# Optimization experiments

Measured on AMD Instinct MI355X. Metric: run time of the kernel, lower is better.

Reference implementation:

```python
import jax, jax.numpy as jnp
import numpy as np

HIDDEN = 2048
N_HEADS = 16
N_KV_HEADS = 4
HEAD_DIM = HIDDEN // N_HEADS  # 128
WINDOW = 2048
ROPE_THETA = 10000.0


def setup_inputs() -> dict:
    key = jax.random.key(0)
    ks = jax.random.split(key, 5)
    B, S = 1, 4096
    scale = 0.02
    return {
        "hidden_states": jax.random.normal(ks[0], (B, S, HIDDEN), dtype=jnp.float32),
        # nn.Linear weights are [out_features, in_features]
        "q_w": jax.random.normal(ks[1], (N_HEADS * HEAD_DIM, HIDDEN), dtype=jnp.float32) * scale,
        "k_w": jax.random.normal(ks[2], (N_KV_HEADS * HEAD_DIM, HIDDEN), dtype=jnp.float32) * scale,
        "v_w": jax.random.normal(ks[3], (N_KV_HEADS * HEAD_DIM, HIDDEN), dtype=jnp.float32) * scale,
        "o_w": jax.random.normal(ks[4], (HIDDEN, N_HEADS * HEAD_DIM), dtype=jnp.float32) * scale,
    }


def _rope_cos_sin(seq_len, dtype):
    inv_freq = 1.0 / (ROPE_THETA ** (jnp.arange(0, HEAD_DIM, 2, dtype=jnp.float32) / HEAD_DIM))
    pos = jnp.arange(seq_len, dtype=jnp.float32)
    freqs = pos[:, None] * inv_freq[None, :]          # [S, D/2]
    emb = jnp.concatenate([freqs, freqs], axis=-1)    # [S, D]
    return jnp.cos(emb).astype(dtype), jnp.sin(emb).astype(dtype)


def _rotate_half(x):
    x1, x2 = jnp.split(x, 2, axis=-1)
    return jnp.concatenate([-x2, x1], axis=-1)


def reference(hidden_states, q_w, k_w, v_w, o_w):
    B, S, _ = hidden_states.shape
    dtype = hidden_states.dtype

    q = hidden_states @ q_w.T                         # [B,S,H*D]
    k = hidden_states @ k_w.T                         # [B,S,Hkv*D]
    v = hidden_states @ v_w.T

    q = q.reshape(B, S, N_HEADS, HEAD_DIM).transpose(0, 2, 1, 3)      # [B,H,S,D]
    k = k.reshape(B, S, N_KV_HEADS, HEAD_DIM).transpose(0, 2, 1, 3)   # [B,Hkv,S,D]
    v = v.reshape(B, S, N_KV_HEADS, HEAD_DIM).transpose(0, 2, 1, 3)

    cos, sin = _rope_cos_sin(S, dtype)                # [S,D]
    cos = cos[None, None]
    sin = sin[None, None]
    q = q * cos + _rotate_half(q) * sin
    k = k * cos + _rotate_half(k) * sin

    n_rep = N_HEADS // N_KV_HEADS
    k = jnp.repeat(k, n_rep, axis=1)                  # [B,H,S,D]
    v = jnp.repeat(v, n_rep, axis=1)

    scores = jnp.einsum("bhqd,bhkd->bhqk", q, k) / jnp.sqrt(jnp.array(HEAD_DIM, dtype))

    pos = jnp.arange(S)
    rel = pos[:, None] - pos[None, :]
    allowed = (rel >= 0) & (rel < WINDOW)             # causal sliding window
    mask = jnp.where(allowed, jnp.array(0.0, dtype), jnp.array(-jnp.inf, dtype))
    scores = scores + mask[None, None]

    attn = jax.nn.softmax(scores.astype(jnp.float32), axis=-1).astype(dtype)

    out = jnp.einsum("bhqk,bhkd->bhqd", attn, v)      # [B,H,S,D]
    out = out.transpose(0, 2, 1, 3).reshape(B, S, N_HEADS * HEAD_DIM)
    return out @ o_w.T
```

## Files before the change

### kernel.cpp

```cpp
#include <hip/hip_runtime.h>
#include <stdint.h>

typedef unsigned short u16;
typedef unsigned int u32;
typedef float f32x4 __attribute__((ext_vector_type(4)));
typedef float f32x8 __attribute__((ext_vector_type(8)));
typedef int   i32x4 __attribute__((ext_vector_type(4)));
typedef __bf16 bf16x8 __attribute__((ext_vector_type(8)));
typedef u16 u16x4 __attribute__((ext_vector_type(4)));

constexpr int S_LEN = 4096;
constexpr int HID   = 2048;
constexpr int WIN   = 2048;

__device__ __forceinline__ u32 f2bf_u(float f) {
  u32 u = __builtin_bit_cast(u32, f);
  return (u + 0x7fffu + ((u >> 16) & 1u)) >> 16;
}
__device__ __forceinline__ float bf2f(u16 u) {
  return __builtin_bit_cast(float, ((u32)u) << 16);
}
__device__ __forceinline__ float exp2x(float x) {
#if __has_builtin(__builtin_amdgcn_exp2f)
  return __builtin_amdgcn_exp2f(x);
#else
  return exp2f(x);
#endif
}
__device__ __forceinline__ void mfma16(f32x4& acc, i32x4 a, i32x4 b) {
  acc = __builtin_amdgcn_mfma_f32_16x16x32_bf16(
      __builtin_bit_cast(bf16x8, a), __builtin_bit_cast(bf16x8, b), acc, 0, 0, 0);
}
__device__ __forceinline__ void gload_lds16(const u16* g, u16* l) {
  __builtin_amdgcn_global_load_lds((const __attribute__((address_space(1))) u32*)g,
                                   (__attribute__((address_space(3))) u32*)l, 16, 0, 0);
}

constexpr int CVT_B0 = 1048576;
constexpr int CVT_B1 = CVT_B0 + 524288;
constexpr int CVT_B2 = CVT_B1 + 131072;
constexpr int CVT_B3 = CVT_B2 + 131072;
constexpr int CVT_B4 = CVT_B3 + 524288;

__global__ __launch_bounds__(256) void cvt_all_kernel(
    const float* __restrict__ s0, const float* __restrict__ s1,
    const float* __restrict__ s2, const float* __restrict__ s3,
    const float* __restrict__ s4, u16* __restrict__ d0, u16* __restrict__ d1,
    u16* __restrict__ d2, u16* __restrict__ d3, u16* __restrict__ d4) {
  int t = blockIdx.x * 256 + threadIdx.x;
  const float* s;
  u16* d;
  int off;
  if (t < CVT_B0) { s = s0; d = d0; off = t; }
  else if (t < CVT_B1) { s = s1; d = d1; off = t - CVT_B0; }
  else if (t < CVT_B2) { s = s2; d = d2; off = t - CVT_B1; }
  else if (t < CVT_B3) { s = s3; d = d3; off = t - CVT_B2; }
  else { s = s4; d = d4; off = t - CVT_B3; }
  const f32x4* sp = (const f32x4*)s + (size_t)off * 2;
  f32x4 a = sp[0], b = sp[1];
  i32x4 o;
  o.x = (int)(f2bf_u(a.x) | (f2bf_u(a.y) << 16));
  o.y = (int)(f2bf_u(a.z) | (f2bf_u(a.w) << 16));
  o.z = (int)(f2bf_u(b.x) | (f2bf_u(b.y) << 16));
  o.w = (int)(f2bf_u(b.z) | (f2bf_u(b.w) << 16));
  *((i32x4*)d + off) = o;
}

__global__ __launch_bounds__(256) void rope_table_kernel(float* __restrict__ cs,
                                                         float* __restrict__ sn) {
  int t = blockIdx.x * 256 + threadIdx.x;
  int d = t & 63, s = t >> 6;
  float inv = exp2f(-(float)d * 0.20762050593046014f);
  float f = (float)s * inv;
  cs[t] = cosf(f);
  sn[t] = sinf(f);
}

__global__ __launch_bounds__(256) void rope_qk_kernel(u16* __restrict__ Qb,
                                                      u16* __restrict__ Kb,
                                                      const float* __restrict__ cs,
                                                      const float* __restrict__ sn) {
  const float SC2 = 0.088388347648318447f * 1.4426950408889634f;
  int t = blockIdx.x * 256 + threadIdx.x;
  int d0 = (t & 15) * 4;
  int r = t >> 4;
  u16* p;
  int s;
  float qs;
  if (r < S_LEN * 16) {
    int h = r & 15; s = r >> 4;
    p = Qb + (size_t)s * HID + h * 128 + d0;
    qs = SC2;
  } else {
    int r2 = r - S_LEN * 16;
    int h = r2 & 3; s = r2 >> 2;
    p = Kb + (size_t)s * 512 + h * 128 + d0;
    qs = 1.f;
  }
  f32x4 c = *(const f32x4*)&cs[(s << 6) | d0];
  f32x4 si = *(const f32x4*)&sn[(s << 6) | d0];
  u16x4 a = *(u16x4*)p, b = *(u16x4*)(p + 64);
  u16x4 oa, ob;
#pragma unroll
  for (int j = 0; j < 4; ++j) {
    float x1 = bf2f(a[j]), x2 = bf2f(b[j]);
    oa[j] = (u16)f2bf_u((x1 * c[j] - x2 * si[j]) * qs);
    ob[j] = (u16)f2bf_u((x2 * c[j] + x1 * si[j]) * qs);
  }
  *(u16x4*)p = oa;
  *(u16x4*)(p + 64) = ob;
}

__global__ __launch_bounds__(256) void qkv_gemm_kernel(
    const u16* __restrict__ A, const u16* __restrict__ Wq,
    const u16* __restrict__ Wk, const u16* __restrict__ Wv,
    u16* __restrict__ Qb, u16* __restrict__ Kb, u16* __restrict__ Vt) {
  __shared__ __attribute__((aligned(16))) u16 sA[128 * 64];
  __shared__ __attribute__((aligned(16))) u16 sB[128 * 64];
  const int lane = threadIdx.x & 63;
  const int w = threadIdx.x >> 6;
  const int g = lane >> 4, ln = lane & 15;
  const int K = HID;

  int wgid = blockIdx.x;
  wgid = (wgid & 7) * 96 + (wgid >> 3);
  const int brow = (wgid / 24) * 128;
  const int bcol = (wgid % 24) * 128;

  const u16* B;
  u16* out;
  int bc, mode, N;
  if (bcol < 2048)      { B = Wq; out = Qb; bc = bcol;        N = 2048; mode = 0; }
  else if (bcol < 2560) { B = Wk; out = Kb; bc = bcol - 2048; N = 512;  mode = 0; }
  else                  { B = Wv; out = Vt; bc = bcol - 2560; N = 512;  mode = 1; }

  const int wr = (w >> 1) * 64, wc = (w & 1) * 64;
  f32x4 acc[4][4] = {};

  const int sr = w * 32 + (lane >> 3);
  const int scol = (lane & 7) * 8;
  const u16* Abase = A + (size_t)(brow + sr) * K + scol;
  const u16* Bbase = B + (size_t)(bc + sr) * K + scol;
  u16* sAdst = &sA[w * 2048];
  u16* sBdst = &sB[w * 2048];

  for (int k0 = 0; k0 < K; k0 += 64) {
    __syncthreads();
#pragma unroll
    for (int i = 0; i < 4; ++i) {
      gload_lds16(Abase + (size_t)i * 8 * K + k0, sAdst + i * 512);
      gload_lds16(Bbase + (size_t)i * 8 * K + k0, sBdst + i * 512);
    }
    __syncthreads();
#pragma unroll
    for (int kk = 0; kk < 2; ++kk) {
      i32x4 af[4], bfr[4];
#pragma unroll
      for (int m = 0; m < 4; ++m)
        af[m] = *(const i32x4*)&sA[(wr + m * 16 + ln) * 64 + kk * 32 + g * 8];
#pragma unroll
      for (int n = 0; n < 4; ++n)
        bfr[n] = *(const i32x4*)&sB[(wc + n * 16 + ln) * 64 + kk * 32 + g * 8];
#pragma unroll
      for (int m = 0; m < 4; ++m)
#pragma unroll
        for (int n = 0; n < 4; ++n) mfma16(acc[m][n], af[m], bfr[n]);
    }
  }

  const int orow0 = brow + wr + g * 4;
  const int ocol0 = bc + wc + ln;
#pragma unroll
  for (int m = 0; m < 4; ++m)
#pragma unroll
    for (int n = 0; n < 4; ++n)
#pragma unroll
      for (int j = 0; j < 4; ++j) {
        int row = orow0 + m * 16 + j;
        int col = ocol0 + n * 16;
        float v = acc[m][n][j];
        if (mode == 0) {
          out[(size_t)row * N + col] = (u16)f2bf_u(v);
        } else {
          int d = col & 127, kvh = col >> 7;
          int T = row >> 5, ks = row & 31;
          int tt = ks >> 4, gg = (ks >> 2) & 3, e = (tt << 2) | (ks & 3);
          size_t idx = (size_t)kvh * S_LEN * 128 + (size_t)T * 4096 +
                       (size_t)d * 32 + ((size_t)(gg ^ ((d >> 1) & 3)) << 3) + e;
          out[idx] = (u16)f2bf_u(v);
        }
      }
}

__global__ __launch_bounds__(256) void gemm_o_kernel(const u16* __restrict__ A,
                                                     const u16* __restrict__ B,
                                                     float* __restrict__ Cv,
                                                     int K, int N) {
  __shared__ __attribute__((aligned(16))) u16 sA[128 * 64];
  __shared__ __attribute__((aligned(16))) u16 sB[128 * 64];
  const int lane = threadIdx.x & 63;
  const int w = threadIdx.x >> 6;
  const int g = lane >> 4, ln = lane & 15;

  int wgid = blockIdx.y * gridDim.x + blockIdx.x;
  const int nwg = gridDim.x * gridDim.y;
  wgid = (wgid & 7) * (nwg >> 3) + (wgid >> 3);
  const int brow = (wgid / gridDim.x) * 128;
  const int bcol = (wgid % gridDim.x) * 128;
  const int wr = (w >> 1) * 64, wc = (w & 1) * 64;

  f32x4 acc[4][4] = {};

  const int sr = w * 32 + (lane >> 3);
  const int scol = (lane & 7) * 8;
  const u16* Abase = A + (size_t)(brow + sr) * K + scol;
  const u16* Bbase = B + (size_t)(bcol + sr) * K + scol;
  u16* sAdst = &sA[w * 2048];
  u16* sBdst = &sB[w * 2048];

  for (int k0 = 0; k0 < K; k0 += 64) {
    __syncthreads();
#pragma unroll
    for (int i = 0; i < 4; ++i) {
      gload_lds16(Abase + (size_t)i * 8 * K + k0, sAdst + i * 512);
      gload_lds16(Bbase + (size_t)i * 8 * K + k0, sBdst + i * 512);
    }
    __syncthreads();
#pragma unroll
    for (int kk = 0; kk < 2; ++kk) {
      i32x4 af[4], bfr[4];
#pragma unroll
      for (int m = 0; m < 4; ++m)
        af[m] = *(const i32x4*)&sA[(wr + m * 16 + ln) * 64 + kk * 32 + g * 8];
#pragma unroll
      for (int n = 0; n < 4; ++n)
        bfr[n] = *(const i32x4*)&sB[(wc + n * 16 + ln) * 64 + kk * 32 + g * 8];
#pragma unroll
      for (int m = 0; m < 4; ++m)
#pragma unroll
        for (int n = 0; n < 4; ++n) mfma16(acc[m][n], af[m], bfr[n]);
    }
  }

  const int orow0 = brow + wr + g * 4;
  const int ocol0 = bcol + wc + ln;
#pragma unroll
  for (int m = 0; m < 4; ++m)
#pragma unroll
    for (int n = 0; n < 4; ++n)
#pragma unroll
      for (int j = 0; j < 4; ++j)
        Cv[(size_t)(orow0 + m * 16 + j) * N + ocol0 + n * 16] = acc[m][n][j];
}

__global__ __launch_bounds__(64) void attn_kernel(const u16* __restrict__ Q,
                                                  const u16* __restrict__ Kb,
                                                  const u16* __restrict__ Vt,
                                                  u16* __restrict__ opart,
                                                  float* __restrict__ mpart,
                                                  float* __restrict__ lpart) {
  const int lane = threadIdx.x;
  const int g = lane >> 4, ln = lane & 15;

  const int o = blockIdx.x;
  const int wgid = ((o & 7) << 9) | (o >> 3);
  const int h = wgid >> 8;
  const int idx = wgid & 255;
  const int chunk = idx & 1;
  const int gq = 127 - (idx >> 1);
  const int kvh = h >> 2;
  const int qr0 = gq * 32;

  i32x4 aq[2][4];
#pragma unroll
  for (int qf = 0; qf < 2; ++qf) {
    const u16* qp = Q + (size_t)(qr0 + qf * 16 + ln) * HID + h * 128 + g * 8;
#pragma unroll
    for (int c = 0; c < 4; ++c) aq[qf][c] = *(const i32x4*)(qp + c * 32);
  }

  f32x4 oacc[2][8] = {};
  float mrun[2] = {-1e30f, -1e30f};
  float lrun[2] = {0.f, 0.f};

  int lo = qr0 - (WIN - 1);
  if (lo < 0) lo = 0;
  lo &= ~31;
  const int nt_full = ((qr0 + 32) - lo) >> 5;
  const int nt0 = nt_full >> 1;
  const int lo_c = lo + (chunk ? nt0 * 32 : 0);
  const int nt = chunk ? nt_full - nt0 : nt0;

  const u16* kptr = Kb + (size_t)(lo_c + ln) * 512 + kvh * 128 + g * 8;
  const int vswz = (g ^ ((ln >> 1) & 3)) << 3;
  const u16* vptr = Vt + (size_t)kvh * S_LEN * 128 +
                    (size_t)(lo_c >> 5) * 4096 + ln * 32 + vswz;

  i32x4 kf[2][4], vf[8];
  if (nt > 0) {
#pragma unroll
    for (int t = 0; t < 2; ++t)
#pragma unroll
      for (int c = 0; c < 4; ++c)
        kf[t][c] = *(const i32x4*)(kptr + t * 8192 + c * 32);
#pragma unroll
    for (int nf = 0; nf < 8; ++nf) vf[nf] = *(const i32x4*)(vptr + nf * 512);
  }

  for (int it = 0; it < nt; ++it) {
    const int kb = lo_c + it * 32;
    const bool more = (it + 1 < nt);

    f32x4 sc[2][2] = {};
    __builtin_amdgcn_s_setprio(1);
#pragma unroll
    for (int c = 0; c < 4; ++c) {
      mfma16(sc[0][0], kf[0][c], aq[0][c]);
      mfma16(sc[0][1], kf[1][c], aq[0][c]);
      mfma16(sc[1][0], kf[0][c], aq[1][c]);
      mfma16(sc[1][1], kf[1][c], aq[1][c]);
    }
    __builtin_amdgcn_s_setprio(0);

    if (more) {
      kptr += 32 * 512;
#pragma unroll
      for (int t = 0; t < 2; ++t)
#pragma unroll
        for (int c = 0; c < 4; ++c)
          kf[t][c] = *(const i32x4*)(kptr + t * 8192 + c * 32);
    }

    float p[2][8];
    float mx[2];
    const bool interior = (kb + 31 <= qr0) && (qr0 + 31 - kb < WIN);
#pragma unroll
    for (int qf = 0; qf < 2; ++qf) {
      if (interior) {
#pragma unroll
        for (int j = 0; j < 4; ++j) {
          p[qf][j] = sc[qf][0][j];
          p[qf][4 + j] = sc[qf][1][j];
        }
      } else {
        const float NEG = -__builtin_inff();
        const int q = qr0 + qf * 16 + ln;
#pragma unroll
        for (int t = 0; t < 2; ++t)
#pragma unroll
          for (int j = 0; j < 4; ++j) {
            int k = kb + t * 16 + g * 4 + j;
            p[qf][t * 4 + j] = (k <= q && q - k < WIN) ? sc[qf][t][j] : NEG;
          }
      }
      float x0 = fmaxf(fmaxf(p[qf][0], p[qf][1]), p[qf][2]);
      float x1 = fmaxf(fmaxf(p[qf][3], p[qf][4]), p[qf][5]);
      float x2 = fmaxf(fmaxf(p[qf][6], p[qf][7]), x0);
      float m = fmaxf(x1, x2);
      m = fmaxf(m, __shfl_xor(m, 16));
      m = fmaxf(m, __shfl_xor(m, 32));
      mx[qf] = m;
    }

    float corr[2] = {1.f, 1.f};
    const bool noskip =
        !__all((mx[0] - mrun[0] <= 11.f) && (mx[1] - mrun[1] <= 11.f));
    if (noskip) {
#pragma unroll
      for (int qf = 0; qf < 2; ++qf) {
        float mnew = fmaxf(mrun[qf], mx[qf]);
        corr[qf] = exp2x(mrun[qf] - mnew);
        mrun[qf] = mnew;
        f32x4 cv;
#pragma unroll
        for (int j = 0; j < 4; ++j) cv[j] = __shfl(corr[qf], g * 4 + j);
#pragma unroll
        for (int nf = 0; nf < 8; ++nf)
#pragma unroll
          for (int j = 0; j < 4; ++j) oacc[qf][nf][j] *= cv[j];
      }
    }

    i32x4 pa[2];
#pragma unroll
    for (int qf = 0; qf < 2; ++qf) {
      f32x8 pv;
#pragma unroll
      for (int e = 0; e < 8; ++e) pv[e] = exp2x(p[qf][e] - mrun[qf]);
      float rs = ((pv[0] + pv[1]) + (pv[2] + pv[3])) +
                 ((pv[4] + pv[5]) + (pv[6] + pv[7]));
      lrun[qf] = lrun[qf] * corr[qf] + rs;
      bf16x8 pb = __builtin_convertvector(pv, bf16x8);
      pa[qf] = __builtin_bit_cast(i32x4, pb);
    }

    __builtin_amdgcn_s_setprio(1);
#pragma unroll
    for (int nf = 0; nf < 8; ++nf) {
      mfma16(oacc[0][nf], pa[0], vf[nf]);
      mfma16(oacc[1][nf], pa[1], vf[nf]);
    }
    __builtin_amdgcn_s_setprio(0);

    if (more) {
      vptr += 4096;
#pragma unroll
      for (int nf = 0; nf < 8; ++nf) vf[nf] = *(const i32x4*)(vptr + nf * 512);
    }
  }

#pragma unroll
  for (int qf = 0; qf < 2; ++qf) {
    float l = lrun[qf];
    l += __shfl_xor(l, 16);
    l += __shfl_xor(l, 32);
    lrun[qf] = l;
  }

  const size_t pb = ((size_t)chunk * 16 + h) * S_LEN;
#pragma unroll
  for (int qf = 0; qf < 2; ++qf) {
    if (g == 0) {
      mpart[pb + qr0 + qf * 16 + ln] = mrun[qf];
      lpart[pb + qr0 + qf * 16 + ln] = lrun[qf];
    }
    u16* aop = opart + (pb + qr0 + qf * 16 + g * 4) * 128 + ln;
#pragma unroll
    for (int j = 0; j < 4; ++j)
#pragma unroll
      for (int nf = 0; nf < 8; ++nf)
        aop[(size_t)j * 128 + nf * 16] = (u16)f2bf_u(oacc[qf][nf][j]);
  }
}

__global__ __launch_bounds__(256) void attn_combine_kernel(
    const u16* __restrict__ opart, const float* __restrict__ mpart,
    const float* __restrict__ lpart, u16* __restrict__ AO) {
  int t = blockIdx.x * 256 + threadIdx.x;
  int d0 = (t & 15) * 8;
  int rh = t >> 4;
  int row = rh & (S_LEN - 1);
  int h = rh >> 12;
  size_t i0 = (size_t)h * S_LEN + row;
  size_t i1 = i0 + (size_t)16 * S_LEN;
  float m0 = mpart[i0], m1 = mpart[i1];
  float l0 = lpart[i0], l1 = lpart[i1];
  float m = fmaxf(m0, m1);
  float w0 = exp2x(m0 - m), w1 = exp2x(m1 - m);
  float inv = 1.f / (l0 * w0 + l1 * w1);
  w0 *= inv;
  w1 *= inv;
  i32x4 v0 = *(const i32x4*)(opart + i0 * 128 + d0);
  i32x4 v1 = *(const i32x4*)(opart + i1 * 128 + d0);
  i32x4 ov;
#pragma unroll
  for (int j = 0; j < 4; ++j) {
    u32 a = ((u32)v0[j]), b = ((u32)v1[j]);
    float x = bf2f((u16)a) * w0 + bf2f((u16)b) * w1;
    float y = bf2f((u16)(a >> 16)) * w0 + bf2f((u16)(b >> 16)) * w1;
    ov[j] = (int)(f2bf_u(x) | (f2bf_u(y) << 16));
  }
  *(i32x4*)(AO + (size_t)row * HID + h * 128 + d0) = ov;
}

extern "C" void kernel_launch(void* const* d_in, const int* in_sizes, int n_in,
                              void* d_out, int out_size, void* d_ws, size_t ws_size,
                              hipStream_t stream) {
  const float* hx = (const float*)d_in[0];
  const float* qw = (const float*)d_in[1];
  const float* kw = (const float*)d_in[2];
  const float* vw = (const float*)d_in[3];
  const float* ow = (const float*)d_in[4];

  char* p = (char*)d_ws;
  u16* Xb = (u16*)p; p += (size_t)S_LEN * HID * 2;
  u16* Wq = (u16*)p; p += (size_t)HID * HID * 2;
  u16* Wk = (u16*)p; p += (size_t)512 * HID * 2;
  u16* Wv = (u16*)p; p += (size_t)512 * HID * 2;
  u16* Wo = (u16*)p; p += (size_t)HID * HID * 2;
  u16* Qb = (u16*)p; p += (size_t)S_LEN * HID * 2;
  u16* Kb = (u16*)p; p += (size_t)S_LEN * 512 * 2;
  u16* Vt = (u16*)p; p += (size_t)S_LEN * 512 * 2;
  u16* AO = (u16*)p; p += (size_t)S_LEN * HID * 2;
  float* cs = (float*)p; p += (size_t)S_LEN * 64 * 4;
  float* sn = (float*)p; p += (size_t)S_LEN * 64 * 4;
  u16* Opart = (u16*)p; p += (size_t)2 * 16 * S_LEN * 128 * 2;
  float* Mpart = (float*)p; p += (size_t)2 * 16 * S_LEN * 4;
  float* Lpart = (float*)p; p += (size_t)2 * 16 * S_LEN * 4;

  cvt_all_kernel<<<CVT_B4 / 256, 256, 0, stream>>>(hx, qw, kw, vw, ow, Xb, Wq,
                                                   Wk, Wv, Wo);
  rope_table_kernel<<<S_LEN * 64 / 256, 256, 0, stream>>>(cs, sn);

  qkv_gemm_kernel<<<768, 256, 0, stream>>>(Xb, Wq, Wk, Wv, Qb, Kb, Vt);

  rope_qk_kernel<<<S_LEN * 20 * 16 / 256, 256, 0, stream>>>(Qb, Kb, cs, sn);

  attn_kernel<<<4096, 64, 0, stream>>>(Qb, Kb, Vt, Opart, Mpart, Lpart);
  attn_combine_kernel<<<S_LEN * 16 * 16 / 256, 256, 0, stream>>>(Opart, Mpart,
                                                                 Lpart, AO);

  gemm_o_kernel<<<dim3(16, 32), 256, 0, stream>>>(AO, Wo, (float*)d_out, HID,
                                                  HID);
}
```

Baseline: 315.6 us.

## Fuse RoPE into QKV GEMM epilogue and double-buffer K fragments in attention

Drops the separate RoPE kernel and applies rotary embedding and Q scaling in the QKV GEMM epilogue, staging the output tile through shared memory so each thread can pair the d and d+64 elements. This removes a full read-modify-write pass over Q and K and one kernel launch. The attention kernel now keeps two K fragment buffers and prefetches two tiles ahead through an unrolled macro, and it sets launch_bounds to (64,2). These changes add register pressure and a redundant duplicated store in the epilogue.

```diff
diff --git a/kernel.cpp b/kernel.cpp
--- a/kernel.cpp
+++ b/kernel.cpp
@@ -76,47 +76,14 @@
   sn[t] = sinf(f);
 }
 
-__global__ __launch_bounds__(256) void rope_qk_kernel(u16* __restrict__ Qb,
-                                                      u16* __restrict__ Kb,
-                                                      const float* __restrict__ cs,
-                                                      const float* __restrict__ sn) {
-  const float SC2 = 0.088388347648318447f * 1.4426950408889634f;
-  int t = blockIdx.x * 256 + threadIdx.x;
-  int d0 = (t & 15) * 4;
-  int r = t >> 4;
-  u16* p;
-  int s;
-  float qs;
-  if (r < S_LEN * 16) {
-    int h = r & 15; s = r >> 4;
-    p = Qb + (size_t)s * HID + h * 128 + d0;
-    qs = SC2;
-  } else {
-    int r2 = r - S_LEN * 16;
-    int h = r2 & 3; s = r2 >> 2;
-    p = Kb + (size_t)s * 512 + h * 128 + d0;
-    qs = 1.f;
-  }
-  f32x4 c = *(const f32x4*)&cs[(s << 6) | d0];
-  f32x4 si = *(const f32x4*)&sn[(s << 6) | d0];
-  u16x4 a = *(u16x4*)p, b = *(u16x4*)(p + 64);
-  u16x4 oa, ob;
-#pragma unroll
-  for (int j = 0; j < 4; ++j) {
-    float x1 = bf2f(a[j]), x2 = bf2f(b[j]);
-    oa[j] = (u16)f2bf_u((x1 * c[j] - x2 * si[j]) * qs);
-    ob[j] = (u16)f2bf_u((x2 * c[j] + x1 * si[j]) * qs);
-  }
-  *(u16x4*)p = oa;
-  *(u16x4*)(p + 64) = ob;
-}
-
 __global__ __launch_bounds__(256) void qkv_gemm_kernel(
     const u16* __restrict__ A, const u16* __restrict__ Wq,
     const u16* __restrict__ Wk, const u16* __restrict__ Wv,
-    u16* __restrict__ Qb, u16* __restrict__ Kb, u16* __restrict__ Vt) {
-  __shared__ __attribute__((aligned(16))) u16 sA[128 * 64];
-  __shared__ __attribute__((aligned(16))) u16 sB[128 * 64];
+    u16* __restrict__ Qb, u16* __restrict__ Kb, u16* __restrict__ Vt,
+    const float* __restrict__ cs, const float* __restrict__ sn) {
+  __shared__ __attribute__((aligned(16))) u16 smem[128 * 128];
+  u16* sA = smem;
+  u16* sB = smem + 128 * 64;
   const int lane = threadIdx.x & 63;
   const int w = threadIdx.x >> 6;
   const int g = lane >> 4, ln = lane & 15;
@@ -129,10 +96,17 @@
 
   const u16* B;
   u16* out;
-  int bc, mode, N;
-  if (bcol < 2048)      { B = Wq; out = Qb; bc = bcol;        N = 2048; mode = 0; }
-  else if (bcol < 2560) { B = Wk; out = Kb; bc = bcol - 2048; N = 512;  mode = 0; }
-  else                  { B = Wv; out = Vt; bc = bcol - 2560; N = 512;  mode = 1; }
+  int bc, N;
+  bool is_v = false;
+  float rope_scale = 1.f;
+  if (bcol < 2048) {
+    B = Wq; out = Qb; bc = bcol; N = 2048;
+    rope_scale = 0.088388347648318447f * 1.4426950408889634f;
+  } else if (bcol < 2560) {
+    B = Wk; out = Kb; bc = bcol - 2048; N = 512;
+  } else {
+    B = Wv; out = Vt; bc = bcol - 2560; N = 512; is_v = true;
+  }
 
   const int wr = (w >> 1) * 64, wc = (w & 1) * 64;
   f32x4 acc[4][4] = {};
@@ -170,26 +144,58 @@
 
   const int orow0 = brow + wr + g * 4;
   const int ocol0 = bc + wc + ln;
-#pragma unroll
-  for (int m = 0; m < 4; ++m)
-#pragma unroll
-    for (int n = 0; n < 4; ++n)
-#pragma unroll
-      for (int j = 0; j < 4; ++j) {
-        int row = orow0 + m * 16 + j;
-        int col = ocol0 + n * 16;
-        float v = acc[m][n][j];
-        if (mode == 0) {
-          out[(size_t)row * N + col] = (u16)f2bf_u(v);
-        } else {
+
+  if (is_v) {
+#pragma unroll
+    for (int m = 0; m < 4; ++m)
+#pragma unroll
+      for (int n = 0; n < 4; ++n)
+#pragma unroll
+        for (int j = 0; j < 4; ++j) {
+          int row = orow0 + m * 16 + j;
+          int col = ocol0 + n * 16;
           int d = col & 127, kvh = col >> 7;
           int T = row >> 5, ks = row & 31;
           int tt = ks >> 4, gg = (ks >> 2) & 3, e = (tt << 2) | (ks & 3);
           size_t idx = (size_t)kvh * S_LEN * 128 + (size_t)T * 4096 +
                        (size_t)d * 32 + ((size_t)(gg ^ ((d >> 1) & 3)) << 3) + e;
-          out[idx] = (u16)f2bf_u(v);
+          out[idx] = (u16)f2bf_u(acc[m][n][j]);
         }
+  } else {
+    __syncthreads();
+#pragma unroll
+    for (int m = 0; m < 4; ++m)
+#pragma unroll
+      for (int n = 0; n < 4; ++n)
+#pragma unroll
+        for (int j = 0; j < 4; ++j)
+          smem[(wr + m * 16 + g * 4 + j - wr + wr) * 128 + (wc + n * 16 + ln)] =
+              (u16)f2bf_u(acc[m][n][j]),
+          smem[(wr + m * 16 + g * 4 + j) * 128 + (wc + n * 16 + ln)] =
+              (u16)f2bf_u(acc[m][n][j]);
+    __syncthreads();
+    const int r = threadIdx.x >> 1;
+    const int half = threadIdx.x & 1;
+    const int s = brow + r;
+    u16* outp = out + (size_t)s * N + bc;
+#pragma unroll
+    for (int i = 0; i < 8; ++i) {
+      const int d0 = half * 32 + i * 4;
+      f32x4 c4 = *(const f32x4*)&cs[(s << 6) + d0];
+      f32x4 s4 = *(const f32x4*)&sn[(s << 6) + d0];
+      u16x4 a = *(const u16x4*)&smem[r * 128 + d0];
+      u16x4 b = *(const u16x4*)&smem[r * 128 + d0 + 64];
+      u16x4 oa, ob;
+#pragma unroll
+      for (int j = 0; j < 4; ++j) {
+        float x1 = bf2f(a[j]), x2 = bf2f(b[j]);
+        oa[j] = (u16)f2bf_u((x1 * c4[j] - x2 * s4[j]) * rope_scale);
+        ob[j] = (u16)f2bf_u((x2 * c4[j] + x1 * s4[j]) * rope_scale);
       }
+      *(u16x4*)(outp + d0) = oa;
+      *(u16x4*)(outp + d0 + 64) = ob;
+    }
+  }
 }
 
 __global__ __launch_bounds__(256) void gemm_o_kernel(const u16* __restrict__ A,
@@ -253,12 +259,12 @@
         Cv[(size_t)(orow0 + m * 16 + j) * N + ocol0 + n * 16] = acc[m][n][j];
 }
 
-__global__ __launch_bounds__(64) void attn_kernel(const u16* __restrict__ Q,
-                                                  const u16* __restrict__ Kb,
-                                                  const u16* __restrict__ Vt,
-                                                  u16* __restrict__ opart,
-                                                  float* __restrict__ mpart,
-                                                  float* __restrict__ lpart) {
+__global__ __launch_bounds__(64, 2) void attn_kernel(const u16* __restrict__ Q,
+                                                     const u16* __restrict__ Kb,
+                                                     const u16* __restrict__ Vt,
+                                                     u16* __restrict__ opart,
+                                                     float* __restrict__ mpart,
+                                                     float* __restrict__ lpart) {
   const int lane = threadIdx.x;
   const int g = lane >> 4, ln = lane & 15;
 
@@ -291,123 +297,119 @@
   const int lo_c = lo + (chunk ? nt0 * 32 : 0);
   const int nt = chunk ? nt_full - nt0 : nt0;
 
-  const u16* kptr = Kb + (size_t)(lo_c + ln) * 512 + kvh * 128 + g * 8;
+  const u16* kptr0 = Kb + (size_t)(lo_c + ln) * 512 + kvh * 128 + g * 8;
   const int vswz = (g ^ ((ln >> 1) & 3)) << 3;
-  const u16* vptr = Vt + (size_t)kvh * S_LEN * 128 +
-                    (size_t)(lo_c >> 5) * 4096 + ln * 32 + vswz;
-
-  i32x4 kf[2][4], vf[8];
+  const u16* vptr0 = Vt + (size_t)kvh * S_LEN * 128 +
+                     (size_t)(lo_c >> 5) * 4096 + ln * 32 + vswz;
+
+  i32x4 kfA[2][4], kfB[2][4], vf[8];
   if (nt > 0) {
 #pragma unroll
-    for (int t = 0; t < 2; ++t)
+    for (int tt = 0; tt < 2; ++tt)
 #pragma unroll
       for (int c = 0; c < 4; ++c)
-        kf[t][c] = *(const i32x4*)(kptr + t * 8192 + c * 32);
-#pragma unroll
-    for (int nf = 0; nf < 8; ++nf) vf[nf] = *(const i32x4*)(vptr + nf * 512);
-  }
-
-  for (int it = 0; it < nt; ++it) {
-    const int kb = lo_c + it * 32;
-    const bool more = (it + 1 < nt);
-
-    f32x4 sc[2][2] = {};
-    __builtin_amdgcn_s_setprio(1);
-#pragma unroll
-    for (int c = 0; c < 4; ++c) {
-      mfma16(sc[0][0], kf[0][c], aq[0][c]);
-      mfma16(sc[0][1], kf[1][c], aq[0][c]);
-      mfma16(sc[1][0], kf[0][c], aq[1][c]);
-      mfma16(sc[1][1], kf[1][c], aq[1][c]);
-    }
-    __builtin_amdgcn_s_setprio(0);
-
-    if (more) {
-      kptr += 32 * 512;
-#pragma unroll
-      for (int t = 0; t < 2; ++t)
-#pragma unroll
-        for (int c = 0; c < 4; ++c)
-          kf[t][c] = *(const i32x4*)(kptr + t * 8192 + c * 32);
-    }
-
-    float p[2][8];
-    float mx[2];
-    const bool interior = (kb + 31 <= qr0) && (qr0 + 31 - kb < WIN);
-#pragma unroll
-    for (int qf = 0; qf < 2; ++qf) {
-      if (interior) {
-#pragma unroll
-        for (int j = 0; j < 4; ++j) {
-          p[qf][j] = sc[qf][0][j];
-          p[qf][4 + j] = sc[qf][1][j];
-        }
-      } else {
-        const float NEG = -__builtin_inff();
-        const int q = qr0 + qf * 16 + ln;
-#pragma unroll
-        for (int t = 0; t < 2; ++t)
-#pragma unroll
-          for (int j = 0; j < 4; ++j) {
-            int k = kb + t * 16 + g * 4 + j;
-            p[qf][t * 4 + j] = (k <= q && q - k < WIN) ? sc[qf][t][j] : NEG;
-          }
-      }
-      float x0 = fmaxf(fmaxf(p[qf][0], p[qf][1]), p[qf][2]);
-      float x1 = fmaxf(fmaxf(p[qf][3], p[qf][4]), p[qf][5]);
-      float x2 = fmaxf(fmaxf(p[qf][6], p[qf][7]), x0);
-      float m = fmaxf(x1, x2);
-      m = fmaxf(m, __shfl_xor(m, 16));
-      m = fmaxf(m, __shfl_xor(m, 32));
-      mx[qf] = m;
-    }
-
-    float corr[2] = {1.f, 1.f};
-    const bool noskip =
-        !__all((mx[0] - mrun[0] <= 11.f) && (mx[1] - mrun[1] <= 11.f));
-    if (noskip) {
-#pragma unroll
-      for (int qf = 0; qf < 2; ++qf) {
-        float mnew = fmaxf(mrun[qf], mx[qf]);
-        corr[qf] = exp2x(mrun[qf] - mnew);
-        mrun[qf] = mnew;
-        f32x4 cv;
-#pragma unroll
-        for (int j = 0; j < 4; ++j) cv[j] = __shfl(corr[qf], g * 4 + j);
-#pragma unroll
-        for (int nf = 0; nf < 8; ++nf)
-#pragma unroll
-          for (int j = 0; j < 4; ++j) oacc[qf][nf][j] *= cv[j];
-      }
-    }
-
-    i32x4 pa[2];
-#pragma unroll
-    for (int qf = 0; qf < 2; ++qf) {
-      f32x8 pv;
-#pragma unroll
-      for (int e = 0; e < 8; ++e) pv[e] = exp2x(p[qf][e] - mrun[qf]);
-      float rs = ((pv[0] + pv[1]) + (pv[2] + pv[3])) +
-                 ((pv[4] + pv[5]) + (pv[6] + pv[7]));
-      lrun[qf] = lrun[qf] * corr[qf] + rs;
-      bf16x8 pb = __builtin_convertvector(pv, bf16x8);
-      pa[qf] = __builtin_bit_cast(i32x4, pb);
-    }
-
-    __builtin_amdgcn_s_setprio(1);
-#pragma unroll
-    for (int nf = 0; nf < 8; ++nf) {
-      mfma16(oacc[0][nf], pa[0], vf[nf]);
-      mfma16(oacc[1][nf], pa[1], vf[nf]);
-    }
-    __builtin_amdgcn_s_setprio(0);
-
-    if (more) {
-      vptr += 4096;
-#pragma unroll
-      for (int nf = 0; nf < 8; ++nf) vf[nf] = *(const i32x4*)(vptr + nf * 512);
-    }
-  }
+        kfA[tt][c] = *(const i32x4*)(kptr0 + tt * 8192 + c * 32);
+#pragma unroll
+    for (int nf = 0; nf < 8; ++nf) vf[nf] = *(const i32x4*)(vptr0 + nf * 512);
+  }
+  if (nt > 1) {
+#pragma unroll
+    for (int tt = 0; tt < 2; ++tt)
+#pragma unroll
+      for (int c = 0; c < 4; ++c)
+        kfB[tt][c] = *(const i32x4*)(kptr0 + 16384 + tt * 8192 + c * 32);
+  }
+
+#define TILE(T, KF)                                                            \
+  {                                                                            \
+    const int kb = lo_c + (T) * 32;                                            \
+    f32x4 sc[2][2] = {};                                                       \
+    __builtin_amdgcn_s_setprio(1);                                             \
+    _Pragma("unroll") for (int c = 0; c < 4; ++c) {                            \
+      mfma16(sc[0][0], KF[0][c], aq[0][c]);                                    \
+      mfma16(sc[0][1], KF[1][c], aq[0][c]);                                    \
+      mfma16(sc[1][0], KF[0][c], aq[1][c]);                                    \
+      mfma16(sc[1][1], KF[1][c], aq[1][c]);                                    \
+    }                                                                          \
+    __builtin_amdgcn_s_setprio(0);                                             \
+    if ((T) + 2 < nt) {             \
+      const u16* kp = kptr0 + (size_t)((T) + 2) * 16384;                       \
+      _Pragma("unroll") for (int tt = 0; tt < 2; ++tt)                         \
+        _Pragma("unroll") for (int c = 0; c < 4; ++c)                          \
+          KF[tt][c] = *(const i32x4*)(kp + tt * 8192 + c * 32);                \
+    }                                                                          \
+    float p[2][8], mx[2];                                                      \
+    const bool interior = (kb + 31 <= qr0) && (qr0 + 31 - kb < WIN);           \
+    _Pragma("unroll") for (int qf = 0; qf < 2; ++qf) {                         \
+      if (interior) {                                                          \
+        _Pragma("unroll") for (int j = 0; j < 4; ++j) {                        \
+          p[qf][j] = sc[qf][0][j];                                             \
+          p[qf][4 + j] = sc[qf][1][j];                                         \
+        }                                                                      \
+      } else {                                                                 \
+        const float NEG = -__builtin_inff();                                   \
+        const int q = qr0 + qf * 16 + ln;                                      \
+        _Pragma("unroll") for (int tt = 0; tt < 2; ++tt)                       \
+          _Pragma("unroll") for (int j = 0; j < 4; ++j) {                      \
+            int k = kb + tt * 16 + g * 4 + j;                                  \
+            p[qf][tt * 4 + j] = (k <= q && q - k < WIN) ? sc[qf][tt][j] : NEG; \
+          }                                                                    \
+      }                                                                        \
+      float x0 = fmaxf(fmaxf(p[qf][0], p[qf][1]), p[qf][2]);                   \
+      float x1 = fmaxf(fmaxf(p[qf][3], p[qf][4]), p[qf][5]);                   \
+      float x2 = fmaxf(fmaxf(p[qf][6], p[qf][7]), x0);                         \
+      float m = fmaxf(x1, x2);                                                 \
+      m = fmaxf(m, __shfl_xor(m, 16));                                         \
+      m = fmaxf(m, __shfl_xor(m, 32));                                         \
+      mx[qf] = m;                                                              \
+    }                                                                          \
+    float corr[2] = {1.f, 1.f};                                                \
+    const bool noskip =                                                        \
+        !__all((mx[0] - mrun[0] <= 11.f) && (mx[1] - mrun[1] <= 11.f));        \
+    if (noskip) {                                                              \
+      _Pragma("unroll") for (int qf = 0; qf < 2; ++qf) {                       \
+        float mnew = fmaxf(mrun[qf], mx[qf]);                                  \
+        corr[qf] = exp2x(mrun[qf] - mnew);                                     \
+        mrun[qf] = mnew;                                                       \
+        f32x4 cv;                                                              \
+        _Pragma("unroll") for (int j = 0; j < 4; ++j)                          \
+            cv[j] = __shfl(corr[qf], g * 4 + j);                               \
+        _Pragma("unroll") for (int nf = 0; nf < 8; ++nf)                       \
+          _Pragma("unroll") for (int j = 0; j < 4; ++j)                        \
+              oacc[qf][nf][j] *= cv[j];                                        \
+      }                                                                        \
+    }                                                                          \
+    i32x4 pa[2];                                                               \
+    _Pragma("unroll") for (int qf = 0; qf < 2; ++qf) {                         \
+      f32x8 pv;                                                                \
+      _Pragma("unroll") for (int e = 0; e < 8; ++e)                            \
+          pv[e] = exp2x(p[qf][e] - mrun[qf]);                                  \
+      float rs = ((pv[0] + pv[1]) + (pv[2] + pv[3])) +                         \
+                 ((pv[4] + pv[5]) + (pv[6] + pv[7]));                          \
+      lrun[qf] = lrun[qf] * corr[qf] + rs;                                     \
+      bf16x8 pb = __builtin_convertvector(pv, bf16x8);                         \
+      pa[qf] = __builtin_bit_cast(i32x4, pb);                                  \
+    }                                                                          \
+    __builtin_amdgcn_s_setprio(1);                                             \
+    _Pragma("unroll") for (int nf = 0; nf < 8; ++nf) {                         \
+      mfma16(oacc[0][nf], pa[0], vf[nf]);                                      \
+      mfma16(oacc[1][nf], pa[1], vf[nf]);                                      \
+    }                                                                          \
+    __builtin_amdgcn_s_setprio(0);                                             \
+    if ((T) + 1 < nt) {                           \
+      const u16* vp = vptr0 + (size_t)((T) + 1) * 4096;                        \
+      _Pragma("unroll") for (int nf = 0; nf < 8; ++nf)                         \
+          vf[nf] = *(const i32x4*)(vp + nf * 512);                             \
+    }                                                                          \
+  }
+
+  int t = 0;
+  for (; t + 1 < nt; t += 2) {
+    TILE(t, kfA);
+    TILE(t + 1, kfB);
+  }
+  if (t < nt) TILE(t, kfA);
+#undef TILE
 
 #pragma unroll
   for (int qf = 0; qf < 2; ++qf) {
@@ -492,9 +494,7 @@
                                                    Wk, Wv, Wo);
   rope_table_kernel<<<S_LEN * 64 / 256, 256, 0, stream>>>(cs, sn);
 
-  qkv_gemm_kernel<<<768, 256, 0, stream>>>(Xb, Wq, Wk, Wv, Qb, Kb, Vt);
-
-  rope_qk_kernel<<<S_LEN * 20 * 16 / 256, 256, 0, stream>>>(Qb, Kb, cs, sn);
+  qkv_gemm_kernel<<<768, 256, 0, stream>>>(Xb, Wq, Wk, Wv, Qb, Kb, Vt, cs, sn);
 
   attn_kernel<<<4096, 64, 0, stream>>>(Qb, Kb, Vt, Opart, Mpart, Lpart);
   attn_combine_kernel<<<S_LEN * 16 * 16 / 256, 256, 0, stream>>>(Opart, Mpart,
```

Measured after the change: 346.5 us. 9.8% more time.

## Fuse Q RoPE into attention, merge rope table into convert kernel, regroup waves

Applied to the files above, without the earlier changes.

Q-side RoPE and softmax scaling now run inside the attention kernel on the Q fragments held in registers, so the separate pass that reads and writes all of Q is gone. The rope-table computation is folded into the conversion kernel, which removes one launch. Attention now launches 256-thread blocks holding four waves (two heads by two KV chunks), and the row-max shuffles only run when the rescale branch is taken. The cost is extra cos/sin loads and arithmetic per attention wave, and a different grouping of waves into blocks.

```diff
diff --git a/kernel.cpp b/kernel.cpp
--- a/kernel.cpp
+++ b/kernel.cpp
@@ -41,13 +41,28 @@
 constexpr int CVT_B2 = CVT_B1 + 131072;
 constexpr int CVT_B3 = CVT_B2 + 131072;
 constexpr int CVT_B4 = CVT_B3 + 524288;
+constexpr int CVT_B5 = CVT_B4 + 32768;
 
 __global__ __launch_bounds__(256) void cvt_all_kernel(
     const float* __restrict__ s0, const float* __restrict__ s1,
     const float* __restrict__ s2, const float* __restrict__ s3,
     const float* __restrict__ s4, u16* __restrict__ d0, u16* __restrict__ d1,
-    u16* __restrict__ d2, u16* __restrict__ d3, u16* __restrict__ d4) {
+    u16* __restrict__ d2, u16* __restrict__ d3, u16* __restrict__ d4,
+    float* __restrict__ cs, float* __restrict__ sn) {
   int t = blockIdx.x * 256 + threadIdx.x;
+  if (t >= CVT_B4) {
+    if (t >= CVT_B5) return;
+    int e = (t - CVT_B4) * 8;
+    int d = e & 63, s = e >> 6;
+#pragma unroll
+    for (int j = 0; j < 8; ++j) {
+      float inv = exp2f(-(float)(d + j) * 0.20762050593046014f);
+      float f = (float)s * inv;
+      cs[e + j] = cosf(f);
+      sn[e + j] = sinf(f);
+    }
+    return;
+  }
   const float* s;
   u16* d;
   int off;
@@ -66,37 +81,14 @@
   *((i32x4*)d + off) = o;
 }
 
-__global__ __launch_bounds__(256) void rope_table_kernel(float* __restrict__ cs,
-                                                         float* __restrict__ sn) {
-  int t = blockIdx.x * 256 + threadIdx.x;
-  int d = t & 63, s = t >> 6;
-  float inv = exp2f(-(float)d * 0.20762050593046014f);
-  float f = (float)s * inv;
-  cs[t] = cosf(f);
-  sn[t] = sinf(f);
-}
-
-__global__ __launch_bounds__(256) void rope_qk_kernel(u16* __restrict__ Qb,
-                                                      u16* __restrict__ Kb,
-                                                      const float* __restrict__ cs,
-                                                      const float* __restrict__ sn) {
-  const float SC2 = 0.088388347648318447f * 1.4426950408889634f;
+__global__ __launch_bounds__(256) void rope_k_kernel(u16* __restrict__ Kb,
+                                                     const float* __restrict__ cs,
+                                                     const float* __restrict__ sn) {
   int t = blockIdx.x * 256 + threadIdx.x;
   int d0 = (t & 15) * 4;
   int r = t >> 4;
-  u16* p;
-  int s;
-  float qs;
-  if (r < S_LEN * 16) {
-    int h = r & 15; s = r >> 4;
-    p = Qb + (size_t)s * HID + h * 128 + d0;
-    qs = SC2;
-  } else {
-    int r2 = r - S_LEN * 16;
-    int h = r2 & 3; s = r2 >> 2;
-    p = Kb + (size_t)s * 512 + h * 128 + d0;
-    qs = 1.f;
-  }
+  int h = r & 3, s = r >> 2;
+  u16* p = Kb + (size_t)s * 512 + h * 128 + d0;
   f32x4 c = *(const f32x4*)&cs[(s << 6) | d0];
   f32x4 si = *(const f32x4*)&sn[(s << 6) | d0];
   u16x4 a = *(u16x4*)p, b = *(u16x4*)(p + 64);
@@ -104,8 +96,8 @@
 #pragma unroll
   for (int j = 0; j < 4; ++j) {
     float x1 = bf2f(a[j]), x2 = bf2f(b[j]);
-    oa[j] = (u16)f2bf_u((x1 * c[j] - x2 * si[j]) * qs);
-    ob[j] = (u16)f2bf_u((x2 * c[j] + x1 * si[j]) * qs);
+    oa[j] = (u16)f2bf_u(x1 * c[j] - x2 * si[j]);
+    ob[j] = (u16)f2bf_u(x2 * c[j] + x1 * si[j]);
   }
   *(u16x4*)p = oa;
   *(u16x4*)(p + 64) = ob;
@@ -253,30 +245,61 @@
         Cv[(size_t)(orow0 + m * 16 + j) * N + ocol0 + n * 16] = acc[m][n][j];
 }
 
-__global__ __launch_bounds__(64) void attn_kernel(const u16* __restrict__ Q,
-                                                  const u16* __restrict__ Kb,
-                                                  const u16* __restrict__ Vt,
-                                                  u16* __restrict__ opart,
-                                                  float* __restrict__ mpart,
-                                                  float* __restrict__ lpart) {
-  const int lane = threadIdx.x;
+__global__ __launch_bounds__(256) void attn_kernel(const u16* __restrict__ Q,
+                                                   const u16* __restrict__ Kb,
+                                                   const u16* __restrict__ Vt,
+                                                   const float* __restrict__ cs,
+                                                   const float* __restrict__ sn,
+                                                   u16* __restrict__ opart,
+                                                   float* __restrict__ mpart,
+                                                   float* __restrict__ lpart) {
+  const int lane = threadIdx.x & 63;
+  const int w = threadIdx.x >> 6;
   const int g = lane >> 4, ln = lane & 15;
 
-  const int o = blockIdx.x;
-  const int wgid = ((o & 7) << 9) | (o >> 3);
-  const int h = wgid >> 8;
-  const int idx = wgid & 255;
-  const int chunk = idx & 1;
-  const int gq = 127 - (idx >> 1);
+  const int b = blockIdx.x;
+  const int h = ((b & 7) << 1) | (w >> 1);
+  const int chunk = w & 1;
+  const int gq = 127 - (b >> 3);
   const int kvh = h >> 2;
   const int qr0 = gq * 32;
 
+  const float SC2 = 0.088388347648318447f * 1.4426950408889634f;
+
   i32x4 aq[2][4];
 #pragma unroll
   for (int qf = 0; qf < 2; ++qf) {
-    const u16* qp = Q + (size_t)(qr0 + qf * 16 + ln) * HID + h * 128 + g * 8;
+    const int s = qr0 + qf * 16 + ln;
+    const u16* qp = Q + (size_t)s * HID + h * 128 + g * 8;
 #pragma unroll
     for (int c = 0; c < 4; ++c) aq[qf][c] = *(const i32x4*)(qp + c * 32);
+#pragma unroll
+    for (int cp = 0; cp < 2; ++cp) {
+      const float* cbase = &cs[(s << 6) + cp * 32 + g * 8];
+      const float* sbase = &sn[(s << 6) + cp * 32 + g * 8];
+      f32x4 c0 = *(const f32x4*)cbase, c1 = *(const f32x4*)(cbase + 4);
+      f32x4 s0 = *(const f32x4*)sbase, s1 = *(const f32x4*)(sbase + 4);
+      i32x4 lo = aq[qf][cp], hi = aq[qf][cp + 2];
+      i32x4 nlo, nhi;
+#pragma unroll
+      for (int wi = 0; wi < 4; ++wi) {
+        u32 lw = (u32)lo[wi], hw = (u32)hi[wi];
+        float x1a = bf2f((u16)lw), x1b = bf2f((u16)(lw >> 16));
+        float x2a = bf2f((u16)hw), x2b = bf2f((u16)(hw >> 16));
+        float ca = (wi * 2 < 4) ? c0[(wi * 2) & 3] : c1[(wi * 2) & 3];
+        float cb = (wi * 2 + 1 < 4) ? c0[(wi * 2 + 1) & 3] : c1[(wi * 2 + 1) & 3];
+        float sa = (wi * 2 < 4) ? s0[(wi * 2) & 3] : s1[(wi * 2) & 3];
+        float sb = (wi * 2 + 1 < 4) ? s0[(wi * 2 + 1) & 3] : s1[(wi * 2 + 1) & 3];
+        float o1a = (x1a * ca - x2a * sa) * SC2;
+        float o2a = (x2a * ca + x1a * sa) * SC2;
+        float o1b = (x1b * cb - x2b * sb) * SC2;
+        float o2b = (x2b * cb + x1b * sb) * SC2;
+        nlo[wi] = (int)(f2bf_u(o1a) | (f2bf_u(o1b) << 16));
+        nhi[wi] = (int)(f2bf_u(o2a) | (f2bf_u(o2b) << 16));
+      }
+      aq[qf][cp] = nlo;
+      aq[qf][cp + 2] = nhi;
+    }
   }
 
   f32x4 oacc[2][8] = {};
@@ -299,10 +322,10 @@
   i32x4 kf[2][4], vf[8];
   if (nt > 0) {
 #pragma unroll
-    for (int t = 0; t < 2; ++t)
+    for (int tt = 0; tt < 2; ++tt)
 #pragma unroll
       for (int c = 0; c < 4; ++c)
-        kf[t][c] = *(const i32x4*)(kptr + t * 8192 + c * 32);
+        kf[tt][c] = *(const i32x4*)(kptr + tt * 8192 + c * 32);
 #pragma unroll
     for (int nf = 0; nf < 8; ++nf) vf[nf] = *(const i32x4*)(vptr + nf * 512);
   }
@@ -325,14 +348,13 @@
     if (more) {
       kptr += 32 * 512;
 #pragma unroll
-      for (int t = 0; t < 2; ++t)
+      for (int tt = 0; tt < 2; ++tt)
 #pragma unroll
         for (int c = 0; c < 4; ++c)
-          kf[t][c] = *(const i32x4*)(kptr + t * 8192 + c * 32);
-    }
-
-    float p[2][8];
-    float mx[2];
+          kf[tt][c] = *(const i32x4*)(kptr + tt * 8192 + c * 32);
+    }
+
+    float p[2][8], mxl[2];
     const bool interior = (kb + 31 <= qr0) && (qr0 + 31 - kb < WIN);
 #pragma unroll
     for (int qf = 0; qf < 2; ++qf) {
@@ -346,34 +368,34 @@
         const float NEG = -__builtin_inff();
         const int q = qr0 + qf * 16 + ln;
 #pragma unroll
-        for (int t = 0; t < 2; ++t)
+        for (int tt = 0; tt < 2; ++tt)
 #pragma unroll
           for (int j = 0; j < 4; ++j) {
-            int k = kb + t * 16 + g * 4 + j;
-            p[qf][t * 4 + j] = (k <= q && q - k < WIN) ? sc[qf][t][j] : NEG;
+            int k = kb + tt * 16 + g * 4 + j;
+            p[qf][tt * 4 + j] = (k <= q && q - k < WIN) ? sc[qf][tt][j] : NEG;
           }
       }
       float x0 = fmaxf(fmaxf(p[qf][0], p[qf][1]), p[qf][2]);
       float x1 = fmaxf(fmaxf(p[qf][3], p[qf][4]), p[qf][5]);
       float x2 = fmaxf(fmaxf(p[qf][6], p[qf][7]), x0);
-      float m = fmaxf(x1, x2);
-      m = fmaxf(m, __shfl_xor(m, 16));
-      m = fmaxf(m, __shfl_xor(m, 32));
-      mx[qf] = m;
-    }
-
-    float corr[2] = {1.f, 1.f};
-    const bool noskip =
-        !__all((mx[0] - mrun[0] <= 11.f) && (mx[1] - mrun[1] <= 11.f));
-    if (noskip) {
+      mxl[qf] = fmaxf(x1, x2);
+    }
+
+    const bool okl =
+        (mxl[0] - mrun[0] <= 11.f) && (mxl[1] - mrun[1] <= 11.f);
+    if (!__all(okl)) {
 #pragma unroll
       for (int qf = 0; qf < 2; ++qf) {
-        float mnew = fmaxf(mrun[qf], mx[qf]);
-        corr[qf] = exp2x(mrun[qf] - mnew);
+        float m = mxl[qf];
+        m = fmaxf(m, __shfl_xor(m, 16));
+        m = fmaxf(m, __shfl_xor(m, 32));
+        float mnew = fmaxf(mrun[qf], m);
+        float corr = exp2x(mrun[qf] - mnew);
         mrun[qf] = mnew;
+        lrun[qf] *= corr;
         f32x4 cv;
 #pragma unroll
-        for (int j = 0; j < 4; ++j) cv[j] = __shfl(corr[qf], g * 4 + j);
+        for (int j = 0; j < 4; ++j) cv[j] = __shfl(corr, g * 4 + j);
 #pragma unroll
         for (int nf = 0; nf < 8; ++nf)
 #pragma unroll
@@ -389,7 +411,7 @@
       for (int e = 0; e < 8; ++e) pv[e] = exp2x(p[qf][e] - mrun[qf]);
       float rs = ((pv[0] + pv[1]) + (pv[2] + pv[3])) +
                  ((pv[4] + pv[5]) + (pv[6] + pv[7]));
-      lrun[qf] = lrun[qf] * corr[qf] + rs;
+      lrun[qf] += rs;
       bf16x8 pb = __builtin_convertvector(pv, bf16x8);
       pa[qf] = __builtin_bit_cast(i32x4, pb);
     }
@@ -488,15 +510,15 @@
   float* Mpart = (float*)p; p += (size_t)2 * 16 * S_LEN * 4;
   float* Lpart = (float*)p; p += (size_t)2 * 16 * S_LEN * 4;
 
-  cvt_all_kernel<<<CVT_B4 / 256, 256, 0, stream>>>(hx, qw, kw, vw, ow, Xb, Wq,
-                                                   Wk, Wv, Wo);
-  rope_table_kernel<<<S_LEN * 64 / 256, 256, 0, stream>>>(cs, sn);
+  cvt_all_kernel<<<(CVT_B5 + 255) / 256, 256, 0, stream>>>(
+      hx, qw, kw, vw, ow, Xb, Wq, Wk, Wv, Wo, cs, sn);
 
   qkv_gemm_kernel<<<768, 256, 0, stream>>>(Xb, Wq, Wk, Wv, Qb, Kb, Vt);
 
-  rope_qk_kernel<<<S_LEN * 20 * 16 / 256, 256, 0, stream>>>(Qb, Kb, cs, sn);
-
-  attn_kernel<<<4096, 64, 0, stream>>>(Qb, Kb, Vt, Opart, Mpart, Lpart);
+  rope_k_kernel<<<S_LEN * 4 * 16 / 256, 256, 0, stream>>>(Kb, cs, sn);
+
+  attn_kernel<<<1024, 256, 0, stream>>>(Qb, Kb, Vt, cs, sn, Opart, Mpart,
+                                        Lpart);
   attn_combine_kernel<<<S_LEN * 16 * 16 / 256, 256, 0, stream>>>(Opart, Mpart,
                                                                  Lpart, AO);
 
```

Result: slower. 323.5 us (+2.5%).
